# Kernel optimization log

Hardware: AMD Instinct MI355X
Metric: run time of the kernel (lower is better)

Reference implementation:

```python
import jax, jax.numpy as jnp
import numpy as np

B, HIDDEN = 16384, 4096
CHUNKS = 4
CHUNK = HIDDEN // CHUNKS          # 1024
LH = max(int(CHUNK * 0.25), 32)   # 256 lstm hidden
LSTM_OUT = 2 * LH                 # bidirectional
TOTAL = CHUNKS * LSTM_OUT         # 2048


def setup_inputs() -> dict:
    key = jax.random.key(0)
    ks = jax.random.split(key, 12)
    s = lambda *sh: 1.0 / np.sqrt(sh[-1])
    return {
        "x": jax.random.normal(ks[0], (B, HIDDEN), jnp.float32),
        # forward-direction LSTM params (PyTorch layout: [4H, in], gate order i,f,g,o)
        "Wih_f": jax.random.normal(ks[1], (4 * LH, CHUNK), jnp.float32) * s(CHUNK),
        "Whh_f": jax.random.normal(ks[2], (4 * LH, LH), jnp.float32) * s(LH),
        "bih_f": jnp.zeros((4 * LH,), jnp.float32),
        "bhh_f": jnp.zeros((4 * LH,), jnp.float32),
        # reverse-direction LSTM params
        "Wih_b": jax.random.normal(ks[3], (4 * LH, CHUNK), jnp.float32) * s(CHUNK),
        "Whh_b": jax.random.normal(ks[4], (4 * LH, LH), jnp.float32) * s(LH),
        "bih_b": jnp.zeros((4 * LH,), jnp.float32),
        "bhh_b": jnp.zeros((4 * LH,), jnp.float32),
        # projection Linear(TOTAL -> HIDDEN) + LayerNorm(HIDDEN)
        "proj_W": jax.random.normal(ks[5], (HIDDEN, TOTAL), jnp.float32) * s(TOTAL),
        "proj_b": jnp.zeros((HIDDEN,), jnp.float32),
        "ln_g": jnp.ones((HIDDEN,), jnp.float32),
        "ln_b": jnp.zeros((HIDDEN,), jnp.float32),
    }


def _lstm_dir(xs, Wih, Whh, bih, bhh):
    """xs: [T, B, C] -> hidden states [T, B, LH]. PyTorch cell math, gates i,f,g,o."""
    Bb = xs.shape[1]
    h0 = jnp.zeros((Bb, LH), xs.dtype)
    c0 = jnp.zeros((Bb, LH), xs.dtype)
    b = bih + bhh

    def step(carry, xt):
        h, c = carry
        gates = xt @ Wih.T + h @ Whh.T + b
        i, f, g, o = jnp.split(gates, 4, axis=-1)
        c = jax.nn.sigmoid(f) * c + jax.nn.sigmoid(i) * jnp.tanh(g)
        h = jax.nn.sigmoid(o) * jnp.tanh(c)
        return (h, c), h

    _, hs = jax.lax.scan(step, (h0, c0), xs)
    return hs


def reference(x, Wih_f, Whh_f, bih_f, bhh_f, Wih_b, Whh_b, bih_b, bhh_b,
              proj_W, proj_b, ln_g, ln_b):
    b = x.shape[0]
    xs = x.reshape(b, CHUNKS, CHUNK).transpose(1, 0, 2)  # [T, B, C]
    hf = _lstm_dir(xs, Wih_f, Whh_f, bih_f, bhh_f)          # [T, B, LH]
    hb = _lstm_dir(xs[::-1], Wih_b, Whh_b, bih_b, bhh_b)[::-1]
    lstm_out = jnp.concatenate([hf, hb], axis=-1)           # [T, B, 2LH]
    flat = lstm_out.transpose(1, 0, 2).reshape(b, TOTAL)    # [B, T*2LH]
    y = flat @ proj_W.T + proj_b
    mu = jnp.mean(y, axis=-1, keepdims=True)
    var = jnp.var(y, axis=-1, keepdims=True)
    y = (y - mu) / jnp.sqrt(var + 1e-5) * ln_g + ln_b
    y = jax.nn.gelu(y, approximate=False)
    return x + y
```

## Files before the change

kernel.cpp:

```cpp
#include <hip/hip_runtime.h>
#include <hip/hip_bf16.h>

#define U16 unsigned short

typedef __attribute__((ext_vector_type(8))) short bf16x8;
typedef __attribute__((ext_vector_type(4))) float f32x4;

__device__ __forceinline__ float bf2f(U16 h) {
  union { unsigned int u; float f; } v; v.u = ((unsigned int)h) << 16; return v.f;
}
__device__ __forceinline__ U16 f2bf(float f) {
  union { float f; unsigned int u; } v; v.f = f;
  unsigned int u = v.u;
  u = (u + 0x7FFFu + ((u >> 16) & 1u)) >> 16;
  return (U16)u;
}
__device__ __forceinline__ float sigm(float x) { return 1.f / (1.f + __expf(-x)); }
__device__ __forceinline__ float tanh_f(float x) {
  x = fminf(10.f, fmaxf(-10.f, x));
  float e = __expf(2.f * x);
  return (e - 1.f) / (e + 1.f);
}

__global__ void cast_bf16_k(const float* __restrict__ src, U16* __restrict__ dst, int n4) {
  int i = blockIdx.x * blockDim.x + threadIdx.x;
  if (i >= n4) return;
  float4 v = ((const float4*)src)[i];
  uint2 o;
  o.x = (unsigned)f2bf(v.x) | ((unsigned)f2bf(v.y) << 16);
  o.y = (unsigned)f2bf(v.z) | ((unsigned)f2bf(v.w) << 16);
  ((uint2*)dst)[i] = o;
}

__global__ void bias_comb_k(const float* __restrict__ a, const float* __restrict__ b,
                            const float* __restrict__ c, const float* __restrict__ d,
                            float* __restrict__ o1, float* __restrict__ o2) {
  int i = blockIdx.x * blockDim.x + threadIdx.x;
  if (i < 1024) { o1[i] = a[i] + b[i]; o2[i] = c[i] + d[i]; }
}

template<bool AF32, bool CF32>
__global__ __launch_bounds__(256) void gemm_bt(
    const void* __restrict__ Av, const U16* __restrict__ Bw,
    void* __restrict__ Cv, int M, int N, int K, const float* __restrict__ bias)
{
  __shared__ __attribute__((aligned(16))) U16 As[8][64][8];
  __shared__ __attribute__((aligned(16))) U16 Bs[8][64][8];
  const int tid = threadIdx.x;
  const int lane = tid & 63, wave = tid >> 6;
  const int wm = wave >> 1, wn = wave & 1;
  const long row0 = (long)blockIdx.y * 128;
  const long col0 = (long)blockIdx.x * 128;

  f32x4 zero = {0.f, 0.f, 0.f, 0.f};
  f32x4 acc[4][4];
#pragma unroll
  for (int mi = 0; mi < 4; ++mi)
#pragma unroll
    for (int ni = 0; ni < 4; ++ni) acc[mi][ni] = zero;

  for (int k0 = 0; k0 < K; k0 += 32) {
    __syncthreads();
    if constexpr (AF32) {
      const float* A = (const float*)Av;
#pragma unroll
      for (int i = 0; i < 4; ++i) {
        int ch = i * 256 + tid;
        int r = ch >> 3, cc = ch & 7;
        const float4 v = *(const float4*)(A + (row0 + r) * (long)K + k0 + cc * 4);
        uint2 o;
        o.x = (unsigned)f2bf(v.x) | ((unsigned)f2bf(v.y) << 16);
        o.y = (unsigned)f2bf(v.z) | ((unsigned)f2bf(v.w) << 16);
        *(uint2*)&As[r >> 4][(cc >> 1) * 16 + (r & 15)][(cc & 1) * 4] = o;
      }
    } else {
      const U16* A = (const U16*)Av;
#pragma unroll
      for (int i = 0; i < 2; ++i) {
        int ch = i * 256 + tid;
        int r = ch >> 2, cc = ch & 3;
        uint4 v = *(const uint4*)(A + (row0 + r) * (long)K + k0 + cc * 8);
        *(uint4*)&As[r >> 4][cc * 16 + (r & 15)][0] = v;
      }
    }
#pragma unroll
    for (int i = 0; i < 2; ++i) {
      int ch = i * 256 + tid;
      int r = ch >> 2, cc = ch & 3;
      uint4 v = *(const uint4*)(Bw + (col0 + r) * (long)K + k0 + cc * 8);
      *(uint4*)&Bs[r >> 4][cc * 16 + (r & 15)][0] = v;
    }
    __syncthreads();
    bf16x8 af[4], bfr[4];
#pragma unroll
    for (int mi = 0; mi < 4; ++mi) af[mi] = *(const bf16x8*)&As[wm * 4 + mi][lane][0];
#pragma unroll
    for (int ni = 0; ni < 4; ++ni) bfr[ni] = *(const bf16x8*)&Bs[wn * 4 + ni][lane][0];
#pragma unroll
    for (int mi = 0; mi < 4; ++mi)
#pragma unroll
      for (int ni = 0; ni < 4; ++ni)
        acc[mi][ni] = __builtin_amdgcn_mfma_f32_16x16x32_bf16(af[mi], bfr[ni], acc[mi][ni], 0, 0, 0);
  }

  const int qa = lane >> 4, ca = lane & 15;
#pragma unroll
  for (int mi = 0; mi < 4; ++mi)
#pragma unroll
    for (int ni = 0; ni < 4; ++ni) {
      long col = col0 + wn * 64 + ni * 16 + ca;
      float bv = 0.f;
      if constexpr (CF32) bv = bias[col];
#pragma unroll
      for (int rr = 0; rr < 4; ++rr) {
        long row = row0 + wm * 64 + mi * 16 + qa * 4 + rr;
        float v = acc[mi][ni][rr];
        if constexpr (CF32) ((float*)Cv)[row * N + col] = v + bv;
        else ((U16*)Cv)[row * N + col] = f2bf(v);
      }
    }
}

__global__ __launch_bounds__(256) void lstm_scan(
    const U16* __restrict__ G, const U16* __restrict__ WhhF,
    const U16* __restrict__ WhhB, const float* __restrict__ biasF,
    const float* __restrict__ biasB, U16* __restrict__ flat)
{
  __shared__ __attribute__((aligned(16))) U16 hbuf[4][8][64][8];
  __shared__ __attribute__((aligned(16))) U16 Bsl[4][8][64][8];
  const int tid = threadIdx.x;
  const int lane = tid & 63, wave = tid >> 6;
  const int qa = lane >> 4, ca = lane & 15;
  const int dir = blockIdx.y;
  const int row0 = blockIdx.x * 64;
  const U16* Whh = dir ? WhhB : WhhF;
  const float* bias = dir ? biasB : biasF;
  const U16* Gd = G + (size_t)dir * (size_t)67108864;

  uint4 z4 = make_uint4(0, 0, 0, 0);
  for (int i = tid; i < 2048; i += 256) ((uint4*)hbuf)[i] = z4;
  __syncthreads();

  float cst[16][4];
#pragma unroll
  for (int u = 0; u < 16; ++u)
#pragma unroll
    for (int r = 0; r < 4; ++r) cst[u][r] = 0.f;

  for (int s = 0; s < 4; ++s) {
    const int t = dir ? (3 - s) : s;
    bf16x8 af[8];
#pragma unroll
    for (int kk = 0; kk < 8; ++kk) af[kk] = *(const bf16x8*)&hbuf[wave][kk][lane][0];

#pragma unroll
    for (int u = 0; u < 16; ++u) {
      __syncthreads();
#pragma unroll
      for (int i = 0; i < 8; ++i) {
        int ch = i * 256 + tid;
        int g = ch >> 9, rem = ch & 511;
        int r = rem >> 5, cc = rem & 31;
        uint4 v = *(const uint4*)(Whh + ((size_t)(g * 256 + u * 16 + r) * 256 + cc * 8));
        *(uint4*)&Bsl[g][cc >> 2][(cc & 3) * 16 + r][0] = v;
      }
      __syncthreads();

      f32x4 acc[4];
#pragma unroll
      for (int g = 0; g < 4; ++g) { f32x4 z = {0.f, 0.f, 0.f, 0.f}; acc[g] = z; }
#pragma unroll
      for (int kk = 0; kk < 8; ++kk)
#pragma unroll
        for (int g = 0; g < 4; ++g)
          acc[g] = __builtin_amdgcn_mfma_f32_16x16x32_bf16(
              af[kk], *(const bf16x8*)&Bsl[g][kk][lane][0], acc[g], 0, 0, 0);

      const int unit = u * 16 + ca;
      const float b0 = bias[unit], b1 = bias[256 + unit], b2 = bias[512 + unit], b3 = bias[768 + unit];
#pragma unroll
      for (int r = 0; r < 4; ++r) {
        int lr = wave * 16 + qa * 4 + r;
        size_t grow = ((size_t)(row0 + lr) * 4 + t) * 1024;
        float gi = acc[0][r] + b0 + bf2f(Gd[grow + unit]);
        float gf = acc[1][r] + b1 + bf2f(Gd[grow + 256 + unit]);
        float gg = acc[2][r] + b2 + bf2f(Gd[grow + 512 + unit]);
        float go = acc[3][r] + b3 + bf2f(Gd[grow + 768 + unit]);
        float c = sigm(gf) * cst[u][r] + sigm(gi) * tanh_f(gg);
        cst[u][r] = c;
        float h = sigm(go) * tanh_f(c);
        U16 hb = f2bf(h);
        hbuf[wave][u >> 1][((u & 1) * 2 + (ca >> 3)) * 16 + qa * 4 + r][ca & 7] = hb;
        flat[(size_t)(row0 + lr) * 2048 + t * 512 + dir * 256 + unit] = hb;
      }
    }
  }
}

__global__ __launch_bounds__(256) void ln_gelu_res(
    const float* __restrict__ y, const float* __restrict__ x,
    const float* __restrict__ lg, const float* __restrict__ lb,
    float* __restrict__ out)
{
  const int row = blockIdx.x, tid = threadIdx.x;
  const float4* yr = (const float4*)(y + (size_t)row * 4096);
  const float4* xr = (const float4*)(x + (size_t)row * 4096);
  float4* outr = (float4*)(out + (size_t)row * 4096);
  const float4* g4 = (const float4*)lg;
  const float4* b4 = (const float4*)lb;
  float4 v[4];
  float s1 = 0.f, s2 = 0.f;
#pragma unroll
  for (int j = 0; j < 4; ++j) {
    float4 t = yr[j * 256 + tid];
    v[j] = t;
    s1 += t.x + t.y + t.z + t.w;
    s2 += t.x * t.x + t.y * t.y + t.z * t.z + t.w * t.w;
  }
#pragma unroll
  for (int off = 32; off > 0; off >>= 1) {
    s1 += __shfl_down(s1, off);
    s2 += __shfl_down(s2, off);
  }
  __shared__ float red[8];
  const int wave = tid >> 6, lane = tid & 63;
  if (lane == 0) { red[wave] = s1; red[4 + wave] = s2; }
  __syncthreads();
  s1 = red[0] + red[1] + red[2] + red[3];
  s2 = red[4] + red[5] + red[6] + red[7];
  const float mu = s1 * (1.f / 4096.f);
  const float rstd = rsqrtf(s2 * (1.f / 4096.f) - mu * mu + 1e-5f);
  const float inv_sqrt2 = 0.70710678118654752f;
#pragma unroll
  for (int j = 0; j < 4; ++j) {
    float4 gg = g4[j * 256 + tid], bb = b4[j * 256 + tid], xx = xr[j * 256 + tid];
    float4 o;
    float tval;
    tval = (v[j].x - mu) * rstd * gg.x + bb.x; o.x = xx.x + 0.5f * tval * (1.f + erff(tval * inv_sqrt2));
    tval = (v[j].y - mu) * rstd * gg.y + bb.y; o.y = xx.y + 0.5f * tval * (1.f + erff(tval * inv_sqrt2));
    tval = (v[j].z - mu) * rstd * gg.z + bb.z; o.z = xx.z + 0.5f * tval * (1.f + erff(tval * inv_sqrt2));
    tval = (v[j].w - mu) * rstd * gg.w + bb.w; o.w = xx.w + 0.5f * tval * (1.f + erff(tval * inv_sqrt2));
    outr[j * 256 + tid] = o;
  }
}

extern "C" void kernel_launch(void* const* d_in, const int* in_sizes, int n_in,
                              void* d_out, int out_size, void* d_ws, size_t ws_size,
                              hipStream_t stream) {
  const float* x      = (const float*)d_in[0];
  const float* Wih_f  = (const float*)d_in[1];
  const float* Whh_f  = (const float*)d_in[2];
  const float* bih_f  = (const float*)d_in[3];
  const float* bhh_f  = (const float*)d_in[4];
  const float* Wih_b  = (const float*)d_in[5];
  const float* Whh_b  = (const float*)d_in[6];
  const float* bih_b  = (const float*)d_in[7];
  const float* bhh_b  = (const float*)d_in[8];
  const float* proj_W = (const float*)d_in[9];
  const float* proj_b = (const float*)d_in[10];
  const float* ln_g   = (const float*)d_in[11];
  const float* ln_b   = (const float*)d_in[12];
  float* out = (float*)d_out;

  char* ws = (char*)d_ws;
  U16*  G    = (U16*)(ws);
  float* y   = (float*)(ws);
  U16*  flat = (U16*)(ws + 268435456);
  U16*  WihF = (U16*)(ws + 335544320);
  U16*  WihB = WihF + 1048576;
  U16*  WhhFb = WihB + 1048576;
  U16*  WhhBb = WhhFb + 262144;
  U16*  PW   = WhhBb + 262144;
  float* biasF = (float*)(PW + 8388608);
  float* biasB = biasF + 1024;

  cast_bf16_k<<<1024, 256, 0, stream>>>(Wih_f, WihF, 262144);
  cast_bf16_k<<<1024, 256, 0, stream>>>(Wih_b, WihB, 262144);
  cast_bf16_k<<<256, 256, 0, stream>>>(Whh_f, WhhFb, 65536);
  cast_bf16_k<<<256, 256, 0, stream>>>(Whh_b, WhhBb, 65536);
  cast_bf16_k<<<8192, 256, 0, stream>>>(proj_W, PW, 2097152);
  bias_comb_k<<<4, 256, 0, stream>>>(bih_f, bhh_f, bih_b, bhh_b, biasF, biasB);

  dim3 g1(8, 512);
  gemm_bt<true, false><<<g1, 256, 0, stream>>>(x, WihF, G, 65536, 1024, 1024, nullptr);
  gemm_bt<true, false><<<g1, 256, 0, stream>>>(x, WihB, G + 67108864, 65536, 1024, 1024, nullptr);

  lstm_scan<<<dim3(256, 2), 256, 0, stream>>>(G, WhhFb, WhhBb, biasF, biasB, flat);

  dim3 g3(32, 128);
  gemm_bt<false, true><<<g3, 256, 0, stream>>>(flat, PW, y, 16384, 4096, 2048, proj_b);

  ln_gelu_res<<<16384, 256, 0, stream>>>(y, x, ln_g, ln_b, out);
}
```

Before: 2.432 ms.

## Pre-pack recurrent weights into MFMA fragment layout and coalesce LSTM output stores

Recurrent weights are pre-packed on the device into the MFMA B-fragment layout, so the scan kernel reads them straight from global memory (L2-resident) instead of staging through shared memory with two barriers per unit step. Biases are folded into the input-projection GEMM epilogue, gate pre-activations are loaded ahead of the MFMAs, and hidden outputs are buffered in registers and written as 16-byte vectors. The projection weight columns are permuted to match the new flat layout. This trades shared-memory staging and syncs for more global/L2 traffic and register pressure, with a launch bound of 2 blocks per SM.

```diff
diff --git a/kernel.cpp b/kernel.cpp
--- a/kernel.cpp
+++ b/kernel.cpp
@@ -37,6 +37,40 @@
                             float* __restrict__ o1, float* __restrict__ o2) {
   int i = blockIdx.x * blockDim.x + threadIdx.x;
   if (i < 1024) { o1[i] = a[i] + b[i]; o2[i] = c[i] + d[i]; }
+}
+
+__global__ void pack_whh_k(const float* __restrict__ Wf, const float* __restrict__ Wb,
+                           U16* __restrict__ Wp) {
+  int i = blockIdx.x * blockDim.x + threadIdx.x;
+  if (i >= 65536) return;
+  int lane = i & 63;
+  int kk = (i >> 6) & 7;
+  int g  = (i >> 9) & 3;
+  int u  = (i >> 11) & 15;
+  int d  = i >> 15;
+  const float* W = d ? Wb : Wf;
+  const float* src = W + (size_t)(g * 256 + u * 16 + (lane & 15)) * 256 + kk * 32 + (lane >> 4) * 8;
+  U16 o[8];
+#pragma unroll
+  for (int j = 0; j < 8; ++j) o[j] = f2bf(src[j]);
+  *(uint4*)(Wp + (size_t)i * 8) = *(uint4*)o;
+}
+
+__global__ void cast_pw_perm_k(const float* __restrict__ src, U16* __restrict__ dst) {
+  int i = blockIdx.x * blockDim.x + threadIdx.x;
+  if (i >= 1048576) return;
+  int kp8 = (i & 255) * 8;
+  int n = i >> 8;
+  const float* row = src + (size_t)n * 2048;
+  U16 o[8];
+#pragma unroll
+  for (int j = 0; j < 8; ++j) {
+    int kp = kp8 + j;
+    int b = kp >> 8, x = kp & 255;
+    int k = b * 256 + (x & 15) * 16 + (x >> 4);
+    o[j] = f2bf(row[k]);
+  }
+  *(uint4*)(dst + (size_t)n * 2048 + kp8) = *(uint4*)o;
 }
 
 template<bool AF32, bool CF32>
@@ -109,37 +143,29 @@
 #pragma unroll
     for (int ni = 0; ni < 4; ++ni) {
       long col = col0 + wn * 64 + ni * 16 + ca;
-      float bv = 0.f;
-      if constexpr (CF32) bv = bias[col];
+      float bv = bias ? bias[col] : 0.f;
 #pragma unroll
       for (int rr = 0; rr < 4; ++rr) {
         long row = row0 + wm * 64 + mi * 16 + qa * 4 + rr;
-        float v = acc[mi][ni][rr];
-        if constexpr (CF32) ((float*)Cv)[row * N + col] = v + bv;
+        float v = acc[mi][ni][rr] + bv;
+        if constexpr (CF32) ((float*)Cv)[row * N + col] = v;
         else ((U16*)Cv)[row * N + col] = f2bf(v);
       }
     }
 }
 
-__global__ __launch_bounds__(256) void lstm_scan(
-    const U16* __restrict__ G, const U16* __restrict__ WhhF,
-    const U16* __restrict__ WhhB, const float* __restrict__ biasF,
-    const float* __restrict__ biasB, U16* __restrict__ flat)
+__global__ __launch_bounds__(256, 2) void lstm_scan2(
+    const U16* __restrict__ G, const U16* __restrict__ Wp,
+    U16* __restrict__ flat)
 {
   __shared__ __attribute__((aligned(16))) U16 hbuf[4][8][64][8];
-  __shared__ __attribute__((aligned(16))) U16 Bsl[4][8][64][8];
   const int tid = threadIdx.x;
   const int lane = tid & 63, wave = tid >> 6;
   const int qa = lane >> 4, ca = lane & 15;
   const int dir = blockIdx.y;
   const int row0 = blockIdx.x * 64;
-  const U16* Whh = dir ? WhhB : WhhF;
-  const float* bias = dir ? biasB : biasF;
-  const U16* Gd = G + (size_t)dir * (size_t)67108864;
-
-  uint4 z4 = make_uint4(0, 0, 0, 0);
-  for (int i = tid; i < 2048; i += 256) ((uint4*)hbuf)[i] = z4;
-  __syncthreads();
+  const U16* Gd = G + (size_t)dir * 67108864u;
+  const U16* Wd = Wp + (size_t)dir * 262144u;
 
   float cst[16][4];
 #pragma unroll
@@ -150,49 +176,63 @@
   for (int s = 0; s < 4; ++s) {
     const int t = dir ? (3 - s) : s;
     bf16x8 af[8];
-#pragma unroll
-    for (int kk = 0; kk < 8; ++kk) af[kk] = *(const bf16x8*)&hbuf[wave][kk][lane][0];
+    if (s == 0) {
+      bf16x8 z = {0, 0, 0, 0, 0, 0, 0, 0};
+#pragma unroll
+      for (int kk = 0; kk < 8; ++kk) af[kk] = z;
+    } else {
+#pragma unroll
+      for (int kk = 0; kk < 8; ++kk) af[kk] = *(const bf16x8*)&hbuf[wave][kk][lane][0];
+    }
+
+    U16 hreg[4][16];
+    const size_t gbase = ((size_t)(row0 + wave * 16 + qa * 4) * 4 + t) * 1024;
 
 #pragma unroll
     for (int u = 0; u < 16; ++u) {
-      __syncthreads();
-#pragma unroll
-      for (int i = 0; i < 8; ++i) {
-        int ch = i * 256 + tid;
-        int g = ch >> 9, rem = ch & 511;
-        int r = rem >> 5, cc = rem & 31;
-        uint4 v = *(const uint4*)(Whh + ((size_t)(g * 256 + u * 16 + r) * 256 + cc * 8));
-        *(uint4*)&Bsl[g][cc >> 2][(cc & 3) * 16 + r][0] = v;
-      }
-      __syncthreads();
-
+      const int unit = u * 16 + ca;
+      U16 gv[4][4];
+#pragma unroll
+      for (int r = 0; r < 4; ++r) {
+        size_t grow = gbase + (size_t)r * 4096;
+        gv[r][0] = Gd[grow + unit];
+        gv[r][1] = Gd[grow + 256 + unit];
+        gv[r][2] = Gd[grow + 512 + unit];
+        gv[r][3] = Gd[grow + 768 + unit];
+      }
+      const U16* Wu = Wd + u * 16384;
       f32x4 acc[4];
 #pragma unroll
       for (int g = 0; g < 4; ++g) { f32x4 z = {0.f, 0.f, 0.f, 0.f}; acc[g] = z; }
 #pragma unroll
-      for (int kk = 0; kk < 8; ++kk)
-#pragma unroll
-        for (int g = 0; g < 4; ++g)
-          acc[g] = __builtin_amdgcn_mfma_f32_16x16x32_bf16(
-              af[kk], *(const bf16x8*)&Bsl[g][kk][lane][0], acc[g], 0, 0, 0);
-
-      const int unit = u * 16 + ca;
-      const float b0 = bias[unit], b1 = bias[256 + unit], b2 = bias[512 + unit], b3 = bias[768 + unit];
+      for (int kk = 0; kk < 8; ++kk) {
+#pragma unroll
+        for (int g = 0; g < 4; ++g) {
+          bf16x8 bfr = *(const bf16x8*)(Wu + g * 4096 + kk * 512 + lane * 8);
+          acc[g] = __builtin_amdgcn_mfma_f32_16x16x32_bf16(af[kk], bfr, acc[g], 0, 0, 0);
+        }
+      }
 #pragma unroll
       for (int r = 0; r < 4; ++r) {
-        int lr = wave * 16 + qa * 4 + r;
-        size_t grow = ((size_t)(row0 + lr) * 4 + t) * 1024;
-        float gi = acc[0][r] + b0 + bf2f(Gd[grow + unit]);
-        float gf = acc[1][r] + b1 + bf2f(Gd[grow + 256 + unit]);
-        float gg = acc[2][r] + b2 + bf2f(Gd[grow + 512 + unit]);
-        float go = acc[3][r] + b3 + bf2f(Gd[grow + 768 + unit]);
+        float gi = acc[0][r] + bf2f(gv[r][0]);
+        float gf = acc[1][r] + bf2f(gv[r][1]);
+        float gg = acc[2][r] + bf2f(gv[r][2]);
+        float go = acc[3][r] + bf2f(gv[r][3]);
         float c = sigm(gf) * cst[u][r] + sigm(gi) * tanh_f(gg);
         cst[u][r] = c;
         float h = sigm(go) * tanh_f(c);
         U16 hb = f2bf(h);
+        hreg[r][u] = hb;
         hbuf[wave][u >> 1][((u & 1) * 2 + (ca >> 3)) * 16 + qa * 4 + r][ca & 7] = hb;
-        flat[(size_t)(row0 + lr) * 2048 + t * 512 + dir * 256 + unit] = hb;
-      }
+      }
+    }
+
+#pragma unroll
+    for (int r = 0; r < 4; ++r) {
+      size_t off = (size_t)(row0 + wave * 16 + qa * 4 + r) * 2048 +
+                   (size_t)t * 512 + (size_t)dir * 256 + (size_t)ca * 16;
+      *(uint4*)(flat + off)     = *(uint4*)&hreg[r][0];
+      *(uint4*)(flat + off + 8) = *(uint4*)&hreg[r][8];
     }
   }
 }
@@ -268,24 +308,22 @@
   U16*  flat = (U16*)(ws + 268435456);
   U16*  WihF = (U16*)(ws + 335544320);
   U16*  WihB = WihF + 1048576;
-  U16*  WhhFb = WihB + 1048576;
-  U16*  WhhBb = WhhFb + 262144;
-  U16*  PW   = WhhBb + 262144;
+  U16*  Wp   = WihB + 1048576;
+  U16*  PW   = Wp + 524288;
   float* biasF = (float*)(PW + 8388608);
   float* biasB = biasF + 1024;
 
   cast_bf16_k<<<1024, 256, 0, stream>>>(Wih_f, WihF, 262144);
   cast_bf16_k<<<1024, 256, 0, stream>>>(Wih_b, WihB, 262144);
-  cast_bf16_k<<<256, 256, 0, stream>>>(Whh_f, WhhFb, 65536);
-  cast_bf16_k<<<256, 256, 0, stream>>>(Whh_b, WhhBb, 65536);
-  cast_bf16_k<<<8192, 256, 0, stream>>>(proj_W, PW, 2097152);
+  pack_whh_k<<<256, 256, 0, stream>>>(Whh_f, Whh_b, Wp);
+  cast_pw_perm_k<<<4096, 256, 0, stream>>>(proj_W, PW);
   bias_comb_k<<<4, 256, 0, stream>>>(bih_f, bhh_f, bih_b, bhh_b, biasF, biasB);
 
   dim3 g1(8, 512);
-  gemm_bt<true, false><<<g1, 256, 0, stream>>>(x, WihF, G, 65536, 1024, 1024, nullptr);
-  gemm_bt<true, false><<<g1, 256, 0, stream>>>(x, WihB, G + 67108864, 65536, 1024, 1024, nullptr);
-
-  lstm_scan<<<dim3(256, 2), 256, 0, stream>>>(G, WhhFb, WhhBb, biasF, biasB, flat);
+  gemm_bt<true, false><<<g1, 256, 0, stream>>>(x, WihF, G, 65536, 1024, 1024, biasF);
+  gemm_bt<true, false><<<g1, 256, 0, stream>>>(x, WihB, G + 67108864, 65536, 1024, 1024, biasB);
+
+  lstm_scan2<<<dim3(256, 2), 256, 0, stream>>>(G, Wp, flat);
 
   dim3 g3(32, 128);
   gemm_bt<false, true><<<g3, 256, 0, stream>>>(flat, PW, y, 16384, 4096, 2048, proj_b);
```

Result: slower. 3.374 ms (+38.8%).
